# Optimization experiments

Measured on AMD Instinct MI355X. Metric: run time of the kernel, lower is better.

Reference implementation:

```python
import jax, jax.numpy as jnp
import numpy as np

HK, DK, HV, DV = 16, 128, 32, 128
VE = (HV // HK) * DV  # 256
CHUNK = 64
KSZ = 4
EPS = 1e-12


def l2_normalize(x):
    sq = jnp.sum(x * x, axis=-1, keepdims=True)
    return x * jax.lax.rsqrt(sq + EPS)


def causal_dwconv_silu(x_bct, w, b):
    # x_bct: [B, C, T]; w: [C, 1, K]; b: [C]; causal depthwise conv then SiLU
    C = x_bct.shape[1]
    y = jax.lax.conv_general_dilated(
        x_bct, w, window_strides=(1,), padding=[(KSZ - 1, 0)],
        dimension_numbers=('NCH', 'OIH', 'NCH'), feature_group_count=C)
    return jax.nn.silu(y + b[None, :, None])


def setup_inputs() -> dict:
    key = jax.random.key(0)
    ks = jax.random.split(key, 12)
    B, T, H = 2, 2048, 2048
    s = 0.02
    return {
        'x': jax.random.normal(ks[0], (B, T, H), jnp.float32),
        'state': jnp.zeros((B, HK, DK, VE), jnp.float32),
        'Wq': jax.random.normal(ks[1], (HK * DK, H), jnp.float32) * s,
        'Wk': jax.random.normal(ks[2], (HK * DK, H), jnp.float32) * s,
        'Wv': jax.random.normal(ks[3], (HV * DV, H), jnp.float32) * s,
        'Wo': jax.random.normal(ks[4], (H, HV * DV), jnp.float32) * s,
        'Wa': jax.random.normal(ks[5], (HK, H), jnp.float32) * s,
        'Wb': jax.random.normal(ks[6], (HK, H), jnp.float32) * s,
        'qcW': jax.random.normal(ks[7], (HK * DK, 1, KSZ), jnp.float32) * 0.3,
        'qcB': jnp.zeros((HK * DK,), jnp.float32),
        'kcW': jax.random.normal(ks[8], (HK * DK, 1, KSZ), jnp.float32) * 0.3,
        'kcB': jnp.zeros((HK * DK,), jnp.float32),
        'vcW': jax.random.normal(ks[9], (HV * DV, 1, KSZ), jnp.float32) * 0.3,
        'vcB': jnp.zeros((HV * DV,), jnp.float32),
    }


def _forward(x, state, Wq, Wk, Wv, Wo, Wa, Wb, qcW, qcB, kcW, kcB, vcW, vcB):
    B, T, H = x.shape
    Cn = CHUNK
    # T is a multiple of CHUNK here (no padding needed)
    nc = T // Cn
    x_bct = jnp.transpose(x, (0, 2, 1))  # [B, H, T]
    # 1x1-conv projections == channelwise linear
    q = causal_dwconv_silu(jnp.einsum('qh,bht->bqt', Wq, x_bct), qcW, qcB)
    k = causal_dwconv_silu(jnp.einsum('qh,bht->bqt', Wk, x_bct), kcW, kcB)
    v = causal_dwconv_silu(jnp.einsum('vh,bht->bvt', Wv, x_bct), vcW, vcB)
    alpha = jax.nn.sigmoid(jnp.einsum('gh,bht->bgt', Wa, x_bct))  # [B,HK,T]
    beta = jax.nn.sigmoid(jnp.einsum('gh,bht->bgt', Wb, x_bct))

    q = jnp.transpose(q, (0, 2, 1)).reshape(B, T, HK, DK)
    k = jnp.transpose(k, (0, 2, 1)).reshape(B, T, HK, DK)
    # regroup value heads by key head: [B,T,HV,DV] -> [B,T,HK,VE]
    v = jnp.transpose(v, (0, 2, 1)).reshape(B, T, HK, VE)
    alpha = jnp.transpose(alpha, (0, 2, 1))  # [B,T,HK]
    beta = jnp.transpose(beta, (0, 2, 1))

    q = l2_normalize(q)
    k = l2_normalize(k)

    # time-major, chunked: [nc, Cn, B, HK, ...]
    def tmchunk(a):
        a = jnp.moveaxis(a, 1, 0)  # [T, B, ...]
        return a.reshape((nc, Cn) + a.shape[1:])

    qc, kc, vc, ac, bc = map(tmchunk, (q, k, v, alpha, beta))

    def step(s, inp):
        qt, kt, vt, at, bt = inp  # qt/kt [B,HK,DK], vt [B,HK,VE], at/bt [B,HK]
        s = s * at[..., None, None]
        retrieved = jnp.einsum('bhkv,bhk->bhv', s, kt)
        err = vt - retrieved
        s = s + bt[..., None, None] * (kt[..., :, None] * err[..., None, :])
        ot = jnp.einsum('bhkv,bhk->bhv', s, qt)
        return s, ot

    @jax.checkpoint
    def chunk_step(s, ch):
        return jax.lax.scan(step, s, ch)

    state, outs = jax.lax.scan(chunk_step, state, (qc, kc, vc, ac, bc))
    # outs: [nc, Cn, B, HK, VE] -> [B, T, HV*DV]
    out = outs.reshape(T, B, HK * VE)
    out = jnp.moveaxis(out, 0, 1)
    out = jnp.einsum('btv,ov->bto', out, Wo)
    return out, state


def reference(x, state, Wq, Wk, Wv, Wo, Wa, Wb, qcW, qcB, kcW, kcB, vcW, vcB):
    return _forward(x, state, Wq, Wk, Wv, Wo, Wa, Wb, qcW, qcB, kcW, kcB, vcW, vcB)
```

## Files before the change

### kernel.cpp

```cpp
#include <hip/hip_runtime.h>
#include <hip/hip_bf16.h>

typedef __attribute__((ext_vector_type(8))) __bf16 bf16x8;
typedef __attribute__((ext_vector_type(8))) short short8;
typedef __attribute__((ext_vector_type(4))) float floatx4;
typedef __attribute__((ext_vector_type(2))) float floatx2;
using u16 = unsigned short;

#define GLOBAL_AS __attribute__((address_space(1)))
#define LDS_AS    __attribute__((address_space(3)))

__device__ __forceinline__ float b2f(u16 u) {
    union { unsigned int i; float f; } v; v.i = ((unsigned int)u) << 16; return v.f;
}
__device__ __forceinline__ u16 f2b(float f) {
    __hip_bfloat16 h = __float2bfloat16(f);
    return __builtin_bit_cast(u16, h);
}
__device__ __forceinline__ float ldf(const void* p, long i, bool isf32) {
    return isf32 ? ((const float*)p)[i] : b2f(((const u16*)p)[i]);
}
__device__ __forceinline__ void gload_lds16(const void* g, void* l) {
    __builtin_amdgcn_global_load_lds((const GLOBAL_AS unsigned int*)g,
                                     (LDS_AS unsigned int*)l, 16, 0, 0);
}
__device__ __forceinline__ float red8(float x) {
    int xi, yi;
    xi = __builtin_bit_cast(int, x);
    yi = __builtin_amdgcn_update_dpp(xi, xi, 0xB1, 0xF, 0xF, false);
    x += __builtin_bit_cast(float, yi);
    xi = __builtin_bit_cast(int, x);
    yi = __builtin_amdgcn_update_dpp(xi, xi, 0x4E, 0xF, 0xF, false);
    x += __builtin_bit_cast(float, yi);
    xi = __builtin_bit_cast(int, x);
    yi = __builtin_amdgcn_update_dpp(xi, xi, 0x141, 0xF, 0xF, false);
    x += __builtin_bit_cast(float, yi);
    return x;
}
__device__ __forceinline__ floatx2 fma2(floatx2 a, floatx2 b, floatx2 c) {
    return __builtin_elementwise_fma(a, b, c);
}
__device__ __forceinline__ void unpack2(int d, float& lo, float& hi) {
    lo = __builtin_bit_cast(float, (int)((unsigned)d << 16));
    hi = __builtin_bit_cast(float, d & 0xffff0000);
}
__device__ __forceinline__ void unpack8(int4 d, float* f) {
    unpack2(d.x, f[0], f[1]); unpack2(d.y, f[2], f[3]);
    unpack2(d.z, f[4], f[5]); unpack2(d.w, f[6], f[7]);
}

__global__ void detect_dtype(const unsigned int* __restrict__ x, int* __restrict__ flag) {
    const int lane = threadIdx.x;
    int sane = 0;
    for (int i = lane; i < 256; i += 64) {
        const unsigned e = (x[i] >> 23) & 0xFF;
        sane += (e >= 100 && e <= 140) ? 1 : 0;
    }
#pragma unroll
    for (int m = 1; m < 64; m <<= 1) sane += __shfl_xor(sane, m, 64);
    if (lane == 0) *flag = (sane >= 128) ? 1 : 0;
}

__global__ __launch_bounds__(256) void cvt_bf16(
    const void* __restrict__ in, u16* __restrict__ out, long n, const int* __restrict__ flag) {
    const bool f32 = (*flag != 0);
    const long i = ((long)blockIdx.x * 256 + threadIdx.x) * 8;
    if (i >= n) return;
    if (f32) {
        const float* p = (const float*)in + i;
        floatx4 a = *(const floatx4*)p, b = *(const floatx4*)(p + 4);
        short8 o;
        o[0] = (short)f2b(a[0]); o[1] = (short)f2b(a[1]);
        o[2] = (short)f2b(a[2]); o[3] = (short)f2b(a[3]);
        o[4] = (short)f2b(b[0]); o[5] = (short)f2b(b[1]);
        o[6] = (short)f2b(b[2]); o[7] = (short)f2b(b[3]);
        *(short8*)(out + i) = o;
    } else {
        *(int4*)(out + i) = *(const int4*)((const u16*)in + i);
    }
}

__global__ __launch_bounds__(256) void gemm_bt128(
    const u16* __restrict__ A, const u16* __restrict__ B, void* __restrict__ C,
    int M, int N, int K, int cmode, const int* __restrict__ flag) {
    const bool c32 = (cmode == 1) || (cmode == 2 && *flag != 0);
    __shared__ __align__(16) u16 As[128 * 32];
    __shared__ __align__(16) u16 Bs[128 * 32];
    const int tid = threadIdx.x, lane = tid & 63, wave = tid >> 6;
    const int bm = blockIdx.y * 128, bn = blockIdx.x * 128;
    const int wm = (wave >> 1) * 64, wn = (wave & 1) * 64;
    const int fr = lane & 15, fq = lane >> 4;
    floatx4 acc[4][4] = {};

    const int srow = tid >> 2, scol = (tid & 3) * 8;
    const long abase = (long)(bm + srow) * K + scol;
    const long bbase = (long)(bn + srow) * K + scol;
    char* lA = (char*)As + (tid & ~63) * 16;
    char* lB = (char*)Bs + (tid & ~63) * 16;

    for (int k0 = 0; k0 < K; k0 += 32) {
        __syncthreads();
        gload_lds16(A + abase + k0, lA);
        gload_lds16(A + abase + (long)64 * K + k0, lA + 4096);
        gload_lds16(B + bbase + k0, lB);
        gload_lds16(B + bbase + (long)64 * K + k0, lB + 4096);
        __syncthreads();
        bf16x8 af[4], bf[4];
#pragma unroll
        for (int i = 0; i < 4; i++) {
            af[i] = __builtin_bit_cast(bf16x8, *(const short8*)&As[(wm + i * 16 + fr) * 32 + fq * 8]);
            bf[i] = __builtin_bit_cast(bf16x8, *(const short8*)&Bs[(wn + i * 16 + fr) * 32 + fq * 8]);
        }
#pragma unroll
        for (int mi = 0; mi < 4; mi++)
#pragma unroll
            for (int ni = 0; ni < 4; ni++)
                acc[mi][ni] = __builtin_amdgcn_mfma_f32_16x16x32_bf16(
                    af[mi], bf[ni], acc[mi][ni], 0, 0, 0);
    }
#pragma unroll
    for (int mi = 0; mi < 4; mi++)
#pragma unroll
        for (int ni = 0; ni < 4; ni++)
#pragma unroll
            for (int r = 0; r < 4; r++) {
                const int m = bm + wm + mi * 16 + fq * 4 + r;
                const int n = bn + wn + ni * 16 + fr;
                const float val = acc[mi][ni][r];
                const long ci = (long)m * N + n;
                if (c32) ((float*)C)[ci] = val;
                else ((u16*)C)[ci] = f2b(val);
            }
}

__global__ __launch_bounds__(256) void ab_gemm(
    const u16* __restrict__ xb, const u16* __restrict__ wab,
    float* __restrict__ alphaT, float* __restrict__ betaT) {
    __shared__ __align__(16) u16 As[64 * 64];
    __shared__ __align__(16) u16 Bs[32 * 64];
    const int tid = threadIdx.x, lane = tid & 63, wave = tid >> 6;
    const int bm = blockIdx.x * 64;
    const int fr = lane & 15, fq = lane >> 4;
    floatx4 acc[2] = {};

    const int srow = tid >> 3, scol = (tid & 7) * 8;
    char* lA = (char*)As + (tid & ~63) * 16;
    char* lB = (char*)Bs + (tid & ~63) * 16;

    for (int k0 = 0; k0 < 2048; k0 += 64) {
        __syncthreads();
        gload_lds16(xb + (long)(bm + srow) * 2048 + k0 + scol, lA);
        gload_lds16(xb + (long)(bm + 32 + srow) * 2048 + k0 + scol, lA + 4096);
        gload_lds16(wab + (long)srow * 2048 + k0 + scol, lB);
        __syncthreads();
#pragma unroll
        for (int ks = 0; ks < 2; ks++) {
            bf16x8 af = __builtin_bit_cast(bf16x8,
                *(const short8*)&As[(wave * 16 + fr) * 64 + ks * 32 + fq * 8]);
#pragma unroll
            for (int nt = 0; nt < 2; nt++) {
                bf16x8 bf = __builtin_bit_cast(bf16x8,
                    *(const short8*)&Bs[(nt * 16 + fr) * 64 + ks * 32 + fq * 8]);
                acc[nt] = __builtin_amdgcn_mfma_f32_16x16x32_bf16(af, bf, acc[nt], 0, 0, 0);
            }
        }
    }
#pragma unroll
    for (int nt = 0; nt < 2; nt++)
#pragma unroll
        for (int r = 0; r < 4; r++) {
            const int m = bm + wave * 16 + fq * 4 + r;
            const int n = nt * 16 + fr;
            const int b = m >> 11, t = m & 2047;
            const float s = 1.f / (1.f + __expf(-acc[nt][r]));
            if (n < 16) alphaT[((long)b * 16 + n) * 2048 + t] = s;
            else betaT[((long)b * 16 + (n - 16)) * 2048 + t] = s;
        }
}

__global__ __launch_bounds__(256) void conv_silu_norm(
    const u16* __restrict__ pre, const void* __restrict__ cw,
    const void* __restrict__ cb, u16* __restrict__ out, const int* __restrict__ flag) {
    const bool f32 = (*flag != 0);
    const int bt = blockIdx.x;
    const int t = bt & 2047;
    const int tid = threadIdx.x;
    const int c0 = tid * 8;
    float y[8];
    float ss = 0.f;
#pragma unroll
    for (int j = 0; j < 8; j++) {
        const int c = c0 + j;
        float acc = ldf(cb, c, f32);
#pragma unroll
        for (int i = 0; i < 4; i++) {
            if (t - 3 + i >= 0)
                acc += ldf(cw, c * 4 + i, f32) * b2f(pre[(long)(bt - 3 + i) * 2048 + c]);
        }
        const float s = acc / (1.f + __expf(-acc));
        y[j] = s;
        ss += s * s;
    }
#pragma unroll
    for (int m = 1; m < 16; m <<= 1) ss += __shfl_xor(ss, m, 64);
    const float inv = rsqrtf(ss + 1e-12f);
#pragma unroll
    for (int j = 0; j < 8; j++) out[(long)bt * 2048 + c0 + j] = f2b(y[j] * inv);
}

__global__ __launch_bounds__(256) void conv_silu_v(
    const u16* __restrict__ pre, const void* __restrict__ cw,
    const void* __restrict__ cb, u16* __restrict__ out, const int* __restrict__ flag) {
    const bool f32 = (*flag != 0);
    const int bt = blockIdx.x;
    const int t = bt & 2047;
    const int tid = threadIdx.x;
    const int c0 = tid * 16;
#pragma unroll
    for (int j = 0; j < 16; j++) {
        const int c = c0 + j;
        float acc = ldf(cb, c, f32);
#pragma unroll
        for (int i = 0; i < 4; i++) {
            if (t - 3 + i >= 0)
                acc += ldf(cw, c * 4 + i, f32) * b2f(pre[(long)(bt - 3 + i) * 4096 + c]);
        }
        out[(long)bt * 4096 + c] = f2b(acc / (1.f + __expf(-acc)));
    }
}

__global__ __launch_bounds__(256) void recurrence_kernel(
    const u16* __restrict__ qn, const u16* __restrict__ kn,
    const u16* __restrict__ vn, const float* __restrict__ alphaT,
    const float* __restrict__ betaT, const void* __restrict__ state_in,
    u16* __restrict__ outs, void* __restrict__ d_out, const int* __restrict__ flag) {
    const bool f32 = (*flag != 0);
    const int blk = blockIdx.x;
    const int vb = blk & 7, h = (blk >> 3) & 15, b = blk >> 7;
    const int tid = threadIdx.x, lane = tid & 63, wave = tid >> 6;
    const int kg = lane & 7, vq = lane >> 3;
    const int vloc = wave * 8 + vq;
    const int vglob = vb * 32 + vloc;

    floatx2 S2[8];
    const long stbase = ((long)(b * 16 + h) * 128 + kg * 16) * 256 + vglob;
#pragma unroll
    for (int p = 0; p < 8; p++) {
        S2[p][0] = ldf(state_in, stbase + (long)(2 * p) * 256, f32);
        S2[p][1] = ldf(state_in, stbase + (long)(2 * p + 1) * 256, f32);
    }

    __shared__ __align__(16) float kf[2][16 * 128];
    __shared__ __align__(16) float qf[2][16 * 128];
    __shared__ __align__(16) float vf[2][16 * 32];

    const int srow = tid >> 4, sc8 = (tid & 15) * 8, vc2 = (tid & 15) * 2;
    const long gkq0 = ((long)b * 2048 + srow) * 2048 + h * 128 + sc8;
    const long gv0  = ((long)b * 2048 + srow) * 4096 + h * 256 + vb * 32 + vc2;
    const long abase = (long)(b * 16 + h) * 2048;

    int4 gk, gq;
    unsigned int gv;
    float ga, gb;

    auto stage_write = [&](int buf) {
        const int kgg = sc8 >> 4, i0 = (sc8 >> 2) & 3;
        float fk[8], fq_[8];
        unpack8(gk, fk);
        unpack8(gq, fq_);
        const int base = srow * 128 + kgg * 4;
        *(floatx4*)&kf[buf][base + i0 * 32]       = floatx4{fk[0], fk[1], fk[2], fk[3]};
        *(floatx4*)&kf[buf][base + (i0 + 1) * 32] = floatx4{fk[4], fk[5], fk[6], fk[7]};
        *(floatx4*)&qf[buf][base + i0 * 32]       = floatx4{fq_[0], fq_[1], fq_[2], fq_[3]};
        *(floatx4*)&qf[buf][base + (i0 + 1) * 32] = floatx4{fq_[4], fq_[5], fq_[6], fq_[7]};
        vf[buf][srow * 32 + vc2]     = b2f((u16)(gv & 0xffffu));
        vf[buf][srow * 32 + vc2 + 1] = b2f((u16)(gv >> 16));
    };

    gk = *(const int4*)(kn + gkq0);
    gq = *(const int4*)(qn + gkq0);
    gv = *(const unsigned int*)(vn + gv0);
    ga = alphaT[abase + (lane & 15)];
    gb = betaT[abase + (lane & 15)];
    stage_write(0);
    __syncthreads();

    for (int c = 0; c < 128; ++c) {
        const int cur = c & 1;
        const float aw = ga, bw = gb;
        if (c + 1 < 128) {
            const long off = (long)(c + 1) * 16 * 2048;
            gk = *(const int4*)(kn + gkq0 + off);
            gq = *(const int4*)(qn + gkq0 + off);
            gv = *(const unsigned int*)(vn + gv0 + (long)(c + 1) * 16 * 4096);
            ga = alphaT[abase + (c + 1) * 16 + (lane & 15)];
            gb = betaT[abase + (c + 1) * 16 + (lane & 15)];
        }

        const float* kfp = kf[cur];
        const float* qfp = qf[cur];
        const float* vfp = vf[cur];
        const long obase = ((long)b * 2048 + c * 16) * 4096 + h * 256 + vglob;

#pragma unroll
        for (int tt = 0; tt < 16; ++tt) {
            floatx2 k2[8], q2[8];
#pragma unroll
            for (int i = 0; i < 4; i++) {
                const floatx4 k4 = *(const floatx4*)&kfp[tt * 128 + i * 32 + kg * 4];
                const floatx4 q4 = *(const floatx4*)&qfp[tt * 128 + i * 32 + kg * 4];
                k2[i * 2]     = __builtin_shufflevector(k4, k4, 0, 1);
                k2[i * 2 + 1] = __builtin_shufflevector(k4, k4, 2, 3);
                q2[i * 2]     = __builtin_shufflevector(q4, q4, 0, 1);
                q2[i * 2 + 1] = __builtin_shufflevector(q4, q4, 2, 3);
            }
            const float vcur = vfp[tt * 32 + vloc];
            const float a = __builtin_bit_cast(float,
                __builtin_amdgcn_readlane(__builtin_bit_cast(int, aw), tt));
            const float bb = __builtin_bit_cast(float,
                __builtin_amdgcn_readlane(__builtin_bit_cast(int, bw), tt));

            floatx2 accA = {0.f, 0.f}, accB = {0.f, 0.f};
#pragma unroll
            for (int p = 0; p < 4; p++) {
                accA = fma2(S2[p], k2[p], accA);
                accB = fma2(S2[4 + p], k2[4 + p], accB);
            }
            const floatx2 accR = accA + accB;
            const float r = red8(accR[0] + accR[1]);
            const float err = fmaf(-a, r, vcur);
            const float cc = bb * err;
            const floatx2 a2 = {a, a}, cc2 = {cc, cc};
            floatx2 oA = {0.f, 0.f}, oB = {0.f, 0.f};
#pragma unroll
            for (int p = 0; p < 4; p++) {
                S2[p] = fma2(cc2, k2[p], a2 * S2[p]);
                S2[4 + p] = fma2(cc2, k2[4 + p], a2 * S2[4 + p]);
                oA = fma2(S2[p], q2[p], oA);
                oB = fma2(S2[4 + p], q2[4 + p], oB);
            }
            const floatx2 accO = oA + oB;
            const float o = red8(accO[0] + accO[1]);
            if (kg == 0)
                outs[obase + (long)tt * 4096] = f2b(o);
        }

        if (c + 1 < 128) stage_write(cur ^ 1);
        __syncthreads();
    }

#pragma unroll
    for (int p = 0; p < 8; p++) {
#pragma unroll
        for (int e = 0; e < 2; e++) {
            const long idx = 8388608L + stbase + (long)(2 * p + e) * 256;
            if (f32) ((float*)d_out)[idx] = S2[p][e];
            else ((u16*)d_out)[idx] = f2b(S2[p][e]);
        }
    }
}

extern "C" void kernel_launch(void* const* d_in, const int* in_sizes, int n_in,
                              void* d_out, int out_size, void* d_ws, size_t ws_size,
                              hipStream_t stream) {
    const void* x   = d_in[0];
    const void* st0 = d_in[1];
    const void* Wq  = d_in[2];
    const void* Wk  = d_in[3];
    const void* Wv  = d_in[4];
    const void* Wo  = d_in[5];
    const void* Wa  = d_in[6];
    const void* Wb  = d_in[7];
    const void* qcW = d_in[8];
    const void* qcB = d_in[9];
    const void* kcW = d_in[10];
    const void* kcB = d_in[11];
    const void* vcW = d_in[12];
    const void* vcB = d_in[13];

    const int M = 4096;
    const long MB = 1024L * 1024L;
    char* w = (char*)d_ws;
    int*   flag   = (int*)w;
    float* alphaT = (float*)(w + 1024);
    float* betaT  = (float*)(w + 1024 + 262144);
    u16*   wab    = (u16*)(w + 1024 + 524288);
    u16* xb    = (u16*)(w + 1 * MB);
    u16* wqb   = (u16*)(w + 17 * MB);
    u16* wkb   = (u16*)(w + 25 * MB);
    u16* wvb   = (u16*)(w + 33 * MB);
    u16* qpreb = (u16*)(w + 49 * MB);
    u16* kpreb = (u16*)(w + 65 * MB);
    u16* vpreb = (u16*)(w + 81 * MB);
    u16* qn    = (u16*)(w + 113 * MB);
    u16* kn    = (u16*)(w + 129 * MB);
    u16* vn    = (u16*)(w + 145 * MB);
    u16* wob   = xb;
    u16* outs  = qpreb;

    dim3 blk(256);
    detect_dtype<<<dim3(1), dim3(64), 0, stream>>>((const unsigned int*)x, flag);

    cvt_bf16<<<dim3(4096), blk, 0, stream>>>(x,  xb,  8388608L, flag);
    cvt_bf16<<<dim3(2048), blk, 0, stream>>>(Wq, wqb, 4194304L, flag);
    cvt_bf16<<<dim3(2048), blk, 0, stream>>>(Wk, wkb, 4194304L, flag);
    cvt_bf16<<<dim3(4096), blk, 0, stream>>>(Wv, wvb, 8388608L, flag);
    cvt_bf16<<<dim3(16),   blk, 0, stream>>>(Wa, wab, 32768L, flag);
    cvt_bf16<<<dim3(16),   blk, 0, stream>>>(Wb, wab + 32768, 32768L, flag);

    gemm_bt128<<<dim3(2048 / 128, M / 128), blk, 0, stream>>>(xb, wqb, qpreb, M, 2048, 2048, 3, flag);
    gemm_bt128<<<dim3(2048 / 128, M / 128), blk, 0, stream>>>(xb, wkb, kpreb, M, 2048, 2048, 3, flag);
    gemm_bt128<<<dim3(4096 / 128, M / 128), blk, 0, stream>>>(xb, wvb, vpreb, M, 4096, 2048, 3, flag);
    ab_gemm<<<dim3(64), blk, 0, stream>>>(xb, wab, alphaT, betaT);

    cvt_bf16<<<dim3(4096), blk, 0, stream>>>(Wo, wob, 8388608L, flag);

    conv_silu_norm<<<dim3(M), blk, 0, stream>>>(qpreb, qcW, qcB, qn, flag);
    conv_silu_norm<<<dim3(M), blk, 0, stream>>>(kpreb, kcW, kcB, kn, flag);
    conv_silu_v<<<dim3(M), blk, 0, stream>>>(vpreb, vcW, vcB, vn, flag);

    recurrence_kernel<<<dim3(256), blk, 0, stream>>>(qn, kn, vn, alphaT, betaT, st0,
                                                     outs, d_out, flag);

    gemm_bt128<<<dim3(2048 / 128, M / 128), blk, 0, stream>>>(outs, wob, d_out, M, 2048, 4096, 2, flag);
}
```

Before: 1.609 ms.

## Fuse QKV projection GEMMs and decouple output dot from state update

The three Q/K/V projection GEMMs are merged into one launch over a concatenated weight (wqb, wkb, wvb assumed contiguous), and a new output mode scatters columns back to the separate q/k/v buffers. In the recurrence, the output o = q·S_new is rewritten algebraically as a·(q·S_old) + cc·(q·k), so all three reductions are computed in one pass before the state update. This removes the serial dependency between the state update and the output reduction and cuts two kernel launches. The cost is an extra k·q dot product per step and a slightly different floating-point summation order.

```diff
diff --git a/kernel.cpp b/kernel.cpp
--- a/kernel.cpp
+++ b/kernel.cpp
@@ -84,6 +84,7 @@
     const u16* __restrict__ A, const u16* __restrict__ B, void* __restrict__ C,
     int M, int N, int K, int cmode, const int* __restrict__ flag) {
     const bool c32 = (cmode == 1) || (cmode == 2 && *flag != 0);
+    const bool qkv = (cmode == 4);
     __shared__ __align__(16) u16 As[128 * 32];
     __shared__ __align__(16) u16 Bs[128 * 32];
     const int tid = threadIdx.x, lane = tid & 63, wave = tid >> 6;
@@ -127,9 +128,18 @@
                 const int m = bm + wm + mi * 16 + fq * 4 + r;
                 const int n = bn + wn + ni * 16 + fr;
                 const float val = acc[mi][ni][r];
-                const long ci = (long)m * N + n;
-                if (c32) ((float*)C)[ci] = val;
-                else ((u16*)C)[ci] = f2b(val);
+                if (qkv) {
+                    u16* base = (u16*)C;
+                    long off;
+                    if (n < 2048)      off = (long)m * 2048 + n;
+                    else if (n < 4096) off = 8388608L + (long)m * 2048 + (n - 2048);
+                    else               off = 16777216L + (long)m * 4096 + (n - 4096);
+                    base[off] = f2b(val);
+                } else {
+                    const long ci = (long)m * N + n;
+                    if (c32) ((float*)C)[ci] = val;
+                    else ((u16*)C)[ci] = f2b(val);
+                }
             }
 }
 
@@ -320,27 +330,31 @@
             const float bb = __builtin_bit_cast(float,
                 __builtin_amdgcn_readlane(__builtin_bit_cast(int, bw), tt));
 
-            floatx2 accA = {0.f, 0.f}, accB = {0.f, 0.f};
+            floatx2 rA = {0.f, 0.f}, rB = {0.f, 0.f};
+            floatx2 sA = {0.f, 0.f}, sB = {0.f, 0.f};
+            floatx2 tA = {0.f, 0.f}, tB = {0.f, 0.f};
 #pragma unroll
             for (int p = 0; p < 4; p++) {
-                accA = fma2(S2[p], k2[p], accA);
-                accB = fma2(S2[4 + p], k2[4 + p], accB);
+                rA = fma2(S2[p], k2[p], rA);
+                rB = fma2(S2[4 + p], k2[4 + p], rB);
+                sA = fma2(S2[p], q2[p], sA);
+                sB = fma2(S2[4 + p], q2[4 + p], sB);
+                tA = fma2(k2[p], q2[p], tA);
+                tB = fma2(k2[4 + p], q2[4 + p], tB);
             }
-            const floatx2 accR = accA + accB;
-            const float r = red8(accR[0] + accR[1]);
+            const floatx2 rS = rA + rB, sS = sA + sB, tS = tA + tB;
+            const float r   = red8(rS[0] + rS[1]);
+            const float rqs = red8(sS[0] + sS[1]);
+            const float rqk = red8(tS[0] + tS[1]);
             const float err = fmaf(-a, r, vcur);
-            const float cc = bb * err;
+            const float cc  = bb * err;
+            const float o = fmaf(cc, rqk, a * rqs);
             const floatx2 a2 = {a, a}, cc2 = {cc, cc};
-            floatx2 oA = {0.f, 0.f}, oB = {0.f, 0.f};
 #pragma unroll
             for (int p = 0; p < 4; p++) {
-                S2[p] = fma2(cc2, k2[p], a2 * S2[p]);
+                S2[p]     = fma2(cc2, k2[p],     a2 * S2[p]);
                 S2[4 + p] = fma2(cc2, k2[4 + p], a2 * S2[4 + p]);
-                oA = fma2(S2[p], q2[p], oA);
-                oB = fma2(S2[4 + p], q2[4 + p], oB);
             }
-            const floatx2 accO = oA + oB;
-            const float o = red8(accO[0] + accO[1]);
             if (kg == 0)
                 outs[obase + (long)tt * 4096] = f2b(o);
         }
@@ -408,9 +422,7 @@
     cvt_bf16<<<dim3(16),   blk, 0, stream>>>(Wa, wab, 32768L, flag);
     cvt_bf16<<<dim3(16),   blk, 0, stream>>>(Wb, wab + 32768, 32768L, flag);
 
-    gemm_bt128<<<dim3(2048 / 128, M / 128), blk, 0, stream>>>(xb, wqb, qpreb, M, 2048, 2048, 3, flag);
-    gemm_bt128<<<dim3(2048 / 128, M / 128), blk, 0, stream>>>(xb, wkb, kpreb, M, 2048, 2048, 3, flag);
-    gemm_bt128<<<dim3(4096 / 128, M / 128), blk, 0, stream>>>(xb, wvb, vpreb, M, 4096, 2048, 3, flag);
+    gemm_bt128<<<dim3(8192 / 128, M / 128), blk, 0, stream>>>(xb, wqb, qpreb, M, 8192, 2048, 4, flag);
     ab_gemm<<<dim3(64), blk, 0, stream>>>(xb, wab, alphaT, betaT);
 
     cvt_bf16<<<dim3(4096), blk, 0, stream>>>(Wo, wob, 8388608L, flag);
```

Result: no change. 1.633 ms (+1.5%).
